# Performance work log

Hardware: AMD Instinct MI355X
Metric: run time of the kernel (lower is better)

Reference implementation:

```python
import jax, jax.numpy as jnp
import numpy as np

NUM_EMBEDDINGS = 512
EMBEDDING_DIM = 64
COMMITMENT_COST = 0.25


def setup_inputs() -> dict:
    key = jax.random.key(0)
    k1, k2 = jax.random.split(key)
    inputs = jax.random.normal(k1, (128, 1024, EMBEDDING_DIM), dtype=jnp.float32)
    embedding = jax.random.normal(k2, (NUM_EMBEDDINGS, EMBEDDING_DIM), dtype=jnp.float32)
    return {"inputs": inputs, "embedding": embedding}


def reference(inputs, embedding):
    """Eval-mode forward of VectorQuantizerEMA.

    Returns (loss, quantized, perplexity, encodings), matching the torch module
    with self.training == False.
    """
    input_shape = inputs.shape
    flat = inputs.reshape(-1, EMBEDDING_DIM)                      # [N, D]
    distances = (
        jnp.sum(flat ** 2, axis=1, keepdims=True)
        + jnp.sum(embedding ** 2, axis=1)
        - 2.0 * flat @ embedding.T
    )
    encoding_indices = jnp.argmin(distances, axis=1)              # [N]
    encodings = jax.nn.one_hot(encoding_indices, NUM_EMBEDDINGS, dtype=jnp.float32)  # [N, K]
    # quantized = onehot @ W  ==  gather rows (same math, cheaper)
    quantized = jnp.take(embedding, encoding_indices, axis=0).reshape(input_shape)

    e_latent_loss = jnp.mean((jax.lax.stop_gradient(quantized) - inputs) ** 2)
    loss = COMMITMENT_COST * e_latent_loss

    # straight-through estimator
    quantized = inputs + jax.lax.stop_gradient(quantized - inputs)

    avg_probs = jnp.mean(encodings, axis=0)                       # [K]
    perplexity = jnp.exp(-jnp.sum(avg_probs * jnp.log(avg_probs + 1e-10)))
    return loss, quantized, perplexity, encodings
```

## Files before the change

kernel.cpp:

```cpp
#include <hip/hip_runtime.h>
#include <math.h>


#define NK 512
#define ND 64
#define NROWS 131072
#define ROWS_PB 64
#define BLOCK 256
#define NBLOCKS (NROWS / ROWS_PB)
#define NTILES 32
#define XSTRIDE 68
#define MARGIN 0.02f

#define Q_OFF    1
#define PERP_OFF 8388609
#define ENC_OFF  8388610

typedef float vf2 __attribute__((ext_vector_type(2)));
typedef float vf4 __attribute__((ext_vector_type(4)));
typedef short vs8 __attribute__((ext_vector_type(8)));

__device__ __forceinline__ unsigned short bf16_rne(float v) {
    union { float f; unsigned int u; } a; a.f = v;
    return (unsigned short)((a.u + 0x7FFFu + ((a.u >> 16) & 1u)) >> 16);
}
__device__ __forceinline__ float bf16_to_f(unsigned short s) {
    union { unsigned int u; float f; } a; a.u = ((unsigned int)s) << 16;
    return a.f;
}

__global__ __launch_bounds__(64) void vq_prep(const float* __restrict__ emb,
                                              float* __restrict__ eknorm,
                                              unsigned int* __restrict__ efrag) {
    const int t = blockIdx.x;
    const int l = threadIdx.x;
    const int c = t * 16 + (l & 15);
    const int quad = l >> 4;
    #pragma unroll
    for (int f = 0; f < 4; ++f) {
        const int kbase = (f & 1) * 32 + quad * 8;
        unsigned int w[4];
        #pragma unroll
        for (int d = 0; d < 4; ++d) {
            float v0 = emb[c * ND + kbase + 2 * d];
            float v1 = emb[c * ND + kbase + 2 * d + 1];
            unsigned short h0 = bf16_rne(v0), h1 = bf16_rne(v1);
            unsigned short l0 = bf16_rne(v0 - bf16_to_f(h0));
            unsigned short l1 = bf16_rne(v1 - bf16_to_f(h1));
            unsigned short e0 = (f < 2) ? h0 : l0;
            unsigned short e1 = (f < 2) ? h1 : l1;
            w[d] = (unsigned int)e0 | ((unsigned int)e1 << 16);
        }
        unsigned int* dst = efrag + ((size_t)(t * 4 + f) * 64 + l) * 4;
        dst[0] = w[0]; dst[1] = w[1]; dst[2] = w[2]; dst[3] = w[3];
    }
    if (quad == 0) {
        const vf4* er = (const vf4*)(emb + c * ND);
        float s0 = 0.f, s1 = 0.f, s2 = 0.f, s3 = 0.f;
        #pragma unroll
        for (int j = 0; j < 16; ++j) {
            vf4 v = er[j];
            s0 += v.x * v.x; s1 += v.y * v.y; s2 += v.z * v.z; s3 += v.w * v.w;
        }
        eknorm[c] = (s0 + s1) + (s2 + s3);
    }
}

__global__ __launch_bounds__(BLOCK) void vq_main(const float* __restrict__ x,
                                                 const float* __restrict__ emb,
                                                 const float* __restrict__ eknorm,
                                                 const unsigned int* __restrict__ efrag,
                                                 float* __restrict__ out,
                                                 int* __restrict__ g_counts,
                                                 float* __restrict__ g_loss) {
    __shared__ float lds_x[ROWS_PB * XSTRIDE];
    __shared__ float ek_lds[NK];
    __shared__ float d1s[ROWS_PB], d2s[ROWS_PB];
    __shared__ int   i1s[ROWS_PB], i2s[ROWS_PB];
    __shared__ int   idx_s[ROWS_PB];
    __shared__ float red[4];

    const int tid  = threadIdx.x;
    const int wave = tid >> 6;
    const int lane = tid & 63;
    const int col  = lane & 15;
    const int quad = lane >> 4;

    {
        const vf4* xp = (const vf4*)(x + (size_t)blockIdx.x * ROWS_PB * ND);
        #pragma unroll
        for (int i = 0; i < 4; ++i) {
            int e4 = tid + i * BLOCK;
            int r  = e4 >> 4;
            int c4 = (e4 & 15) * 4;
            *(vf4*)&lds_x[r * XSTRIDE + c4] = xp[e4];
        }
        ek_lds[tid] = eknorm[tid];
        ek_lds[tid + 256] = eknorm[tid + 256];
    }
    __syncthreads();

    const int arow = wave * 16 + col;
    vs8 ah0, ah1, al0, al1;
    {
        const float* xr = &lds_x[arow * XSTRIDE];
        #pragma unroll
        for (int j = 0; j < 8; ++j) {
            float va = xr[quad * 8 + j];
            float vb = xr[32 + quad * 8 + j];
            unsigned short ha = bf16_rne(va);
            unsigned short hb = bf16_rne(vb);
            ah0[j] = (short)ha; al0[j] = (short)bf16_rne(va - bf16_to_f(ha));
            ah1[j] = (short)hb; al1[j] = (short)bf16_rne(vb - bf16_to_f(hb));
        }
    }

    float d1[4], d2[4];
    int   i1[4], i2[4];
    #pragma unroll
    for (int r = 0; r < 4; ++r) { d1[r] = INFINITY; d2[r] = INFINITY; i1[r] = 0x7FFFFFFF; i2[r] = 0x7FFFFFFF; }

    const vs8* bbase = (const vs8*)efrag;
    vs8 b0 = bbase[0 * 64 + lane];
    vs8 b1 = bbase[1 * 64 + lane];
    vs8 b2 = bbase[2 * 64 + lane];
    vs8 b3 = bbase[3 * 64 + lane];

    for (int t = 0; t < NTILES; ++t) {
        vs8 n0, n1, n2, n3;
        if (t + 1 < NTILES) {
            n0 = bbase[((t + 1) * 4 + 0) * 64 + lane];
            n1 = bbase[((t + 1) * 4 + 1) * 64 + lane];
            n2 = bbase[((t + 1) * 4 + 2) * 64 + lane];
            n3 = bbase[((t + 1) * 4 + 3) * 64 + lane];
        }
        vf4 acc0 = {0.f, 0.f, 0.f, 0.f};
        vf4 acc1 = {0.f, 0.f, 0.f, 0.f};
        acc0 = __builtin_amdgcn_mfma_f32_16x16x32_bf16(ah0, b0, acc0, 0, 0, 0);
        acc1 = __builtin_amdgcn_mfma_f32_16x16x32_bf16(ah1, b1, acc1, 0, 0, 0);
        acc0 = __builtin_amdgcn_mfma_f32_16x16x32_bf16(al0, b0, acc0, 0, 0, 0);
        acc1 = __builtin_amdgcn_mfma_f32_16x16x32_bf16(al1, b1, acc1, 0, 0, 0);
        acc0 = __builtin_amdgcn_mfma_f32_16x16x32_bf16(ah0, b2, acc0, 0, 0, 0);
        acc1 = __builtin_amdgcn_mfma_f32_16x16x32_bf16(ah1, b3, acc1, 0, 0, 0);

        const float ek = ek_lds[t * 16 + col];
        const int cidx = t * 16 + col;
        #pragma unroll
        for (int r = 0; r < 4; ++r) {
            float d = ek - 2.f * (acc0[r] + acc1[r]);
            bool lt1 = d < d1[r];
            bool lt2 = d < d2[r];
            float nd2 = lt1 ? d1[r] : (lt2 ? d : d2[r]);
            int   ni2 = lt1 ? i1[r] : (lt2 ? cidx : i2[r]);
            d2[r] = nd2; i2[r] = ni2;
            d1[r] = lt1 ? d : d1[r];
            i1[r] = lt1 ? cidx : i1[r];
        }
        b0 = n0; b1 = n1; b2 = n2; b3 = n3;
    }

    #pragma unroll
    for (int m = 8; m >= 1; m >>= 1) {
        #pragma unroll
        for (int r = 0; r < 4; ++r) {
            float od1 = __shfl_xor(d1[r], m);
            int   oi1 = __shfl_xor(i1[r], m);
            float od2 = __shfl_xor(d2[r], m);
            int   oi2 = __shfl_xor(i2[r], m);
            bool aF = (d1[r] < od1) || (d1[r] == od1 && i1[r] < oi1);
            float n1 = aF ? d1[r] : od1;  int ni1 = aF ? i1[r] : oi1;
            float ca = aF ? od1 : d1[r];  int cia = aF ? oi1 : i1[r];
            float cb = aF ? d2[r] : od2;  int cib = aF ? i2[r] : oi2;
            bool bF = (cb < ca) || (cb == ca && cib < cia);
            float n2 = bF ? cb : ca;      int ni2 = bF ? cib : cia;
            d1[r] = n1; i1[r] = ni1; d2[r] = n2; i2[r] = ni2;
        }
    }
    if (col == 0) {
        #pragma unroll
        for (int r = 0; r < 4; ++r) {
            int lr = wave * 16 + quad * 4 + r;
            d1s[lr] = d1[r]; i1s[lr] = i1[r];
            d2s[lr] = d2[r]; i2s[lr] = i2[r];
        }
    }

    float* ebase = out + ENC_OFF + (size_t)blockIdx.x * (ROWS_PB * NK);
    {
        if (tid == 0) {
            vf2 z2 = {0.f, 0.f};
            __builtin_nontemporal_store(z2, (vf2*)ebase);
            __builtin_nontemporal_store(z2, (vf2*)(ebase + ROWS_PB * NK - 2));
        }
        vf4 z4 = {0.f, 0.f, 0.f, 0.f};
        float* v4base = ebase + 2;
        #pragma unroll 8
        for (int i = 0; i < 32; ++i) {
            int p = tid + i * BLOCK;
            if (p < 8191) __builtin_nontemporal_store(z4, (vf4*)(v4base + 4 * p));
        }
    }
    __syncthreads();

    if (tid < ROWS_PB) {
        int am = i1s[tid];
        if (d2s[tid] - d1s[tid] < MARGIN) {
            int ia = i1s[tid], ib = i2s[tid];
            const float* xr = &lds_x[tid * XSTRIDE];
            float da, db;
            {
                const vf4* er = (const vf4*)(emb + ia * ND);
                float s0 = 0.f, s1 = 0.f, s2 = 0.f, s3 = 0.f;
                #pragma unroll
                for (int j = 0; j < 16; ++j) {
                    vf4 v = er[j];
                    s0 += xr[4 * j] * v.x; s1 += xr[4 * j + 1] * v.y;
                    s2 += xr[4 * j + 2] * v.z; s3 += xr[4 * j + 3] * v.w;
                }
                da = ek_lds[ia] - 2.f * ((s0 + s1) + (s2 + s3));
            }
            {
                const vf4* er = (const vf4*)(emb + ib * ND);
                float s0 = 0.f, s1 = 0.f, s2 = 0.f, s3 = 0.f;
                #pragma unroll
                for (int j = 0; j < 16; ++j) {
                    vf4 v = er[j];
                    s0 += xr[4 * j] * v.x; s1 += xr[4 * j + 1] * v.y;
                    s2 += xr[4 * j + 2] * v.z; s3 += xr[4 * j + 3] * v.w;
                }
                db = ek_lds[ib] - 2.f * ((s0 + s1) + (s2 + s3));
            }
            am = ((db < da) || (db == da && ib < ia)) ? ib : ia;
        }
        idx_s[tid] = am;
        atomicAdd(&g_counts[am], 1);
    }
    __syncthreads();

    float lacc = 0.f;
    {
        float* qout = out + Q_OFF + (size_t)blockIdx.x * ROWS_PB * ND;
        #pragma unroll 4
        for (int i = 0; i < 16; ++i) {
            int p = tid + i * BLOCK;
            int r = p >> 6;
            int c = p & 63;
            float q = emb[idx_s[r] * ND + c];
            float xv = lds_x[r * XSTRIDE + c];
            __builtin_nontemporal_store(q, &qout[p]);
            float dlt = q - xv;
            lacc += dlt * dlt;
        }
    }

    if (tid < ROWS_PB) {
        ebase[tid * NK + idx_s[tid]] = 1.0f;
    }

    #pragma unroll
    for (int off = 32; off >= 1; off >>= 1) lacc += __shfl_down(lacc, off);
    if (lane == 0) red[wave] = lacc;
    __syncthreads();
    if (tid == 0) atomicAdd(g_loss, (red[0] + red[1]) + (red[2] + red[3]));
}

__global__ __launch_bounds__(512) void vq_final(const int* __restrict__ g_counts,
                                                const float* __restrict__ g_loss,
                                                float* __restrict__ out) {
    __shared__ float red[8];
    int t = threadIdx.x;
    float p = (float)g_counts[t] * (1.0f / (float)NROWS);
    float h = p * logf(p + 1e-10f);
    #pragma unroll
    for (int off = 32; off >= 1; off >>= 1) h += __shfl_down(h, off);
    if ((t & 63) == 0) red[t >> 6] = h;
    __syncthreads();
    if (t == 0) {
        float s = 0.f;
        #pragma unroll
        for (int i = 0; i < 8; ++i) s += red[i];
        out[PERP_OFF] = expf(-s);
        out[0] = 0.25f * g_loss[0] / (float)(NROWS * ND);
    }
}

extern "C" void kernel_launch(void* const* d_in, const int* in_sizes, int n_in,
                              void* d_out, int out_size, void* d_ws, size_t ws_size,
                              hipStream_t stream) {
    const float* x   = (const float*)d_in[0];
    const float* emb = (const float*)d_in[1];
    float* out = (float*)d_out;

    int*          g_counts = (int*)d_ws;
    float*        g_loss   = (float*)((char*)d_ws + 2048);
    float*        eknorm   = (float*)((char*)d_ws + 4096);
    unsigned int* efrag    = (unsigned int*)((char*)d_ws + 8192);

    (void)hipMemsetAsync(d_ws, 0, 4096, stream);

    vq_prep<<<NTILES, 64, 0, stream>>>(emb, eknorm, efrag);
    vq_main<<<NBLOCKS, BLOCK, 0, stream>>>(x, emb, eknorm, efrag, out, g_counts, g_loss);
    vq_final<<<1, 512, 0, stream>>>(g_counts, g_loss, out);
}
```

Measured before the change: 392.8 us.

## Split VQ into argmin sweep and output-write kernels, compute loss from distances

Splits the main kernel into two: a sweep kernel that computes the argmin indices, stores them to workspace and accumulates the loss as |x|^2 plus the best distance, and a separate write kernel that gathers quantized rows and writes the full one-hot encodings directly, replacing the earlier zero-fill followed by a scattered store of ones. The goal is to take the large output-write traffic out of the compute kernel and avoid writing the encodings region twice. The cost is an extra launch, a round trip for indices through global memory, and a loss that now relies on the bf16-based distance plus an fp32 refinement rather than the exact (q-x)^2. The write kernel also switches from nontemporal to plain stores.

```diff
diff --git a/kernel.cpp b/kernel.cpp
--- a/kernel.cpp
+++ b/kernel.cpp
@@ -66,19 +66,17 @@
     }
 }
 
-__global__ __launch_bounds__(BLOCK) void vq_main(const float* __restrict__ x,
-                                                 const float* __restrict__ emb,
-                                                 const float* __restrict__ eknorm,
-                                                 const unsigned int* __restrict__ efrag,
-                                                 float* __restrict__ out,
-                                                 int* __restrict__ g_counts,
-                                                 float* __restrict__ g_loss) {
+__global__ __launch_bounds__(BLOCK) void vq_sweep(const float* __restrict__ x,
+                                                  const float* __restrict__ emb,
+                                                  const float* __restrict__ eknorm,
+                                                  const unsigned int* __restrict__ efrag,
+                                                  int* __restrict__ idx_g,
+                                                  int* __restrict__ g_counts,
+                                                  float* __restrict__ g_loss) {
     __shared__ float lds_x[ROWS_PB * XSTRIDE];
     __shared__ float ek_lds[NK];
     __shared__ float d1s[ROWS_PB], d2s[ROWS_PB];
     __shared__ int   i1s[ROWS_PB], i2s[ROWS_PB];
-    __shared__ int   idx_s[ROWS_PB];
-    __shared__ float red[4];
 
     const int tid  = threadIdx.x;
     const int wave = tid >> 6;
@@ -184,27 +182,12 @@
             d2s[lr] = d2[r]; i2s[lr] = i2[r];
         }
     }
-
-    float* ebase = out + ENC_OFF + (size_t)blockIdx.x * (ROWS_PB * NK);
-    {
-        if (tid == 0) {
-            vf2 z2 = {0.f, 0.f};
-            __builtin_nontemporal_store(z2, (vf2*)ebase);
-            __builtin_nontemporal_store(z2, (vf2*)(ebase + ROWS_PB * NK - 2));
-        }
-        vf4 z4 = {0.f, 0.f, 0.f, 0.f};
-        float* v4base = ebase + 2;
-        #pragma unroll 8
-        for (int i = 0; i < 32; ++i) {
-            int p = tid + i * BLOCK;
-            if (p < 8191) __builtin_nontemporal_store(z4, (vf4*)(v4base + 4 * p));
-        }
-    }
     __syncthreads();
 
     if (tid < ROWS_PB) {
         int am = i1s[tid];
-        if (d2s[tid] - d1s[tid] < MARGIN) {
+        float dfin = d1s[tid];
+        if (d2s[tid] - dfin < MARGIN) {
             int ia = i1s[tid], ib = i2s[tid];
             const float* xr = &lds_x[tid * XSTRIDE];
             float da, db;
@@ -230,38 +213,90 @@
                 }
                 db = ek_lds[ib] - 2.f * ((s0 + s1) + (s2 + s3));
             }
-            am = ((db < da) || (db == da && ib < ia)) ? ib : ia;
-        }
-        idx_s[tid] = am;
+            bool useB = (db < da) || (db == da && ib < ia);
+            am   = useB ? ib : ia;
+            dfin = useB ? db : da;
+        }
+        idx_g[blockIdx.x * ROWS_PB + tid] = am;
         atomicAdd(&g_counts[am], 1);
-    }
+
+        float xn = 0.f;
+        {
+            const float* xr = &lds_x[tid * XSTRIDE];
+            float s0 = 0.f, s1 = 0.f, s2 = 0.f, s3 = 0.f;
+            #pragma unroll
+            for (int j = 0; j < 16; ++j) {
+                s0 += xr[4 * j] * xr[4 * j];         s1 += xr[4 * j + 1] * xr[4 * j + 1];
+                s2 += xr[4 * j + 2] * xr[4 * j + 2]; s3 += xr[4 * j + 3] * xr[4 * j + 3];
+            }
+            xn = (s0 + s1) + (s2 + s3);
+        }
+        float lossv = xn + dfin;
+        #pragma unroll
+        for (int off = 32; off >= 1; off >>= 1) lossv += __shfl_down(lossv, off);
+        if (tid == 0) atomicAdd(g_loss, lossv);
+    }
+}
+
+__global__ __launch_bounds__(BLOCK) void vq_write(const float* __restrict__ emb,
+                                                  const int* __restrict__ idx_g,
+                                                  float* __restrict__ out) {
+    __shared__ int idx_s[ROWS_PB];
+    const int tid = threadIdx.x;
+    if (tid < ROWS_PB) idx_s[tid] = idx_g[blockIdx.x * ROWS_PB + tid];
     __syncthreads();
 
-    float lacc = 0.f;
     {
-        float* qout = out + Q_OFF + (size_t)blockIdx.x * ROWS_PB * ND;
-        #pragma unroll 4
+        float* qout = out + Q_OFF + (size_t)blockIdx.x * (ROWS_PB * ND);
+        #pragma unroll
         for (int i = 0; i < 16; ++i) {
             int p = tid + i * BLOCK;
-            int r = p >> 6;
-            int c = p & 63;
-            float q = emb[idx_s[r] * ND + c];
-            float xv = lds_x[r * XSTRIDE + c];
-            __builtin_nontemporal_store(q, &qout[p]);
-            float dlt = q - xv;
-            lacc += dlt * dlt;
-        }
-    }
-
-    if (tid < ROWS_PB) {
-        ebase[tid * NK + idx_s[tid]] = 1.0f;
-    }
-
-    #pragma unroll
-    for (int off = 32; off >= 1; off >>= 1) lacc += __shfl_down(lacc, off);
-    if (lane == 0) red[wave] = lacc;
-    __syncthreads();
-    if (tid == 0) atomicAdd(g_loss, (red[0] + red[1]) + (red[2] + red[3]));
+            qout[p] = emb[idx_s[p >> 6] * ND + (p & 63)];
+        }
+    }
+
+    float* ebase = out + ENC_OFF + (size_t)blockIdx.x * (ROWS_PB * NK);
+    if (tid == 0) {
+        int a0 = idx_s[0];
+        vf2 h; h.x = (a0 == 0) ? 1.f : 0.f; h.y = (a0 == 1) ? 1.f : 0.f;
+        *(vf2*)ebase = h;
+        int a63 = idx_s[63];
+        vf2 tl; tl.x = (a63 == 510) ? 1.f : 0.f; tl.y = (a63 == 511) ? 1.f : 0.f;
+        *(vf2*)(ebase + ROWS_PB * NK - 2) = tl;
+    }
+    const int c0 = (2 + 4 * tid) & 511;
+    const int rb = (2 + 4 * tid) >> 9;
+    if (c0 != 510) {
+        #pragma unroll
+        for (int i = 0; i < 32; ++i) {
+            int p = tid + i * BLOCK;
+            if (p < 8191) {
+                int am = idx_s[rb + 2 * i];
+                vf4 v;
+                v.x = (am == c0)     ? 1.f : 0.f;
+                v.y = (am == c0 + 1) ? 1.f : 0.f;
+                v.z = (am == c0 + 2) ? 1.f : 0.f;
+                v.w = (am == c0 + 3) ? 1.f : 0.f;
+                *(vf4*)(ebase + 2 + 4 * (size_t)p) = v;
+            }
+        }
+    } else {
+        #pragma unroll
+        for (int i = 0; i < 32; ++i) {
+            int p = tid + i * BLOCK;
+            if (p < 8191) {
+                int r0 = rb + 2 * i;
+                int am0 = idx_s[r0];
+                int am1 = idx_s[r0 + 1];
+                vf4 v;
+                v.x = (am0 == 510) ? 1.f : 0.f;
+                v.y = (am0 == 511) ? 1.f : 0.f;
+                v.z = (am1 == 0)   ? 1.f : 0.f;
+                v.w = (am1 == 1)   ? 1.f : 0.f;
+                *(vf4*)(ebase + 2 + 4 * (size_t)p) = v;
+            }
+        }
+    }
 }
 
 __global__ __launch_bounds__(512) void vq_final(const int* __restrict__ g_counts,
@@ -295,10 +330,12 @@
     float*        g_loss   = (float*)((char*)d_ws + 2048);
     float*        eknorm   = (float*)((char*)d_ws + 4096);
     unsigned int* efrag    = (unsigned int*)((char*)d_ws + 8192);
+    int*          idx_g    = (int*)((char*)d_ws + 8192 + 131072);
 
     (void)hipMemsetAsync(d_ws, 0, 4096, stream);
 
     vq_prep<<<NTILES, 64, 0, stream>>>(emb, eknorm, efrag);
-    vq_main<<<NBLOCKS, BLOCK, 0, stream>>>(x, emb, eknorm, efrag, out, g_counts, g_loss);
+    vq_sweep<<<NBLOCKS, BLOCK, 0, stream>>>(x, emb, eknorm, efrag, idx_g, g_counts, g_loss);
+    vq_write<<<NBLOCKS, BLOCK, 0, stream>>>(emb, idx_g, out);
     vq_final<<<1, 512, 0, stream>>>(g_counts, g_loss, out);
 }
```

Measured after the change: 442.2 us. 12.6% more time.
